# Optimization experiments

Hardware: AMD Instinct MI355X
Metric: run time of the kernel (lower is better)

## Reference

```python
import jax, jax.numpy as jnp
import numpy as np

N_QUBITS = 8
DIM = 2 ** N_QUBITS  # 256


def _apply_1q(state, U, q):
    """Apply a single-qubit gate U on wire q. state: (B, 256) complex64.
    U: (2,2) shared gate or (B,2,2) per-sample gate."""
    B = state.shape[0]
    s = state.reshape(B, 2 ** q, 2, 2 ** (N_QUBITS - 1 - q))
    if U.ndim == 2:
        s = jnp.einsum('ij,bajc->baic', U, s)
    else:
        s = jnp.einsum('bij,bajc->baic', U, s)
    return s.reshape(B, DIM)


def _apply_cnot(state, c, t):
    """CNOT with control wire c, target wire t (pure permutation of amplitudes)."""
    B = state.shape[0]
    a, b = (c, t) if c < t else (t, c)
    s = state.reshape(B, 2 ** a, 2, 2 ** (b - a - 1), 2, 2 ** (N_QUBITS - 1 - b))
    if c < t:
        s0 = s[:, :, 0]                       # control=0: unchanged
        s1 = jnp.flip(s[:, :, 1], axis=3)     # control=1: flip target axis
        s = jnp.stack([s0, s1], axis=2)
    else:
        s0 = s[:, :, :, :, 0]
        s1 = jnp.flip(s[:, :, :, :, 1], axis=2)
        s = jnp.stack([s0, s1], axis=4)
    return s.reshape(B, DIM)


def _rx_batch(theta):
    """Batched RX(theta): (B,) -> (B,2,2) complex64."""
    c = jnp.cos(theta / 2).astype(jnp.complex64)
    s = (-1j * jnp.sin(theta / 2)).astype(jnp.complex64)
    return jnp.stack([jnp.stack([c, s], -1), jnp.stack([s, c], -1)], -2)


def _rot(phi, theta, omega):
    """PennyLane Rot(phi,theta,omega) = RZ(omega) RY(theta) RZ(phi) as a 2x2 matrix."""
    c = jnp.cos(theta / 2)
    s = jnp.sin(theta / 2)
    m00 = jnp.exp(-0.5j * (phi + omega)) * c
    m01 = -jnp.exp(0.5j * (phi - omega)) * s
    m10 = jnp.exp(-0.5j * (phi - omega)) * s
    m11 = jnp.exp(0.5j * (phi + omega)) * c
    return jnp.stack([jnp.stack([m00, m01]), jnp.stack([m10, m11])]).astype(jnp.complex64)


def _circuit(x, weights):
    """AngleEmbedding (RX) + StronglyEntanglingLayers, return <Z_i> per wire: (B,8)."""
    B = x.shape[0]
    state = jnp.zeros((B, DIM), jnp.complex64).at[:, 0].set(1.0)
    # AngleEmbedding: RX(x[:, q]) on wire q
    for q in range(N_QUBITS):
        state = _apply_1q(state, _rx_batch(x[:, q]), q)
    n_layers = weights.shape[0]
    for l in range(n_layers):
        for q in range(N_QUBITS):
            state = _apply_1q(state, _rot(weights[l, q, 0], weights[l, q, 1], weights[l, q, 2]), q)
        r = (l % (N_QUBITS - 1)) + 1  # PennyLane default ranges
        for q in range(N_QUBITS):
            state = _apply_cnot(state, q, (q + r) % N_QUBITS)
    probs = state.real ** 2 + state.imag ** 2  # (B, 256)
    bits = (jnp.arange(DIM)[:, None] >> jnp.arange(N_QUBITS - 1, -1, -1)[None, :]) & 1
    signs = (1.0 - 2.0 * bits).astype(probs.dtype)  # (256, 8); wire 0 = MSB
    return probs @ signs  # (B, 8) expectation values of PauliZ


def setup_inputs() -> dict:
    key = jax.random.key(0)
    k1, k2, k3 = jax.random.split(key, 3)
    B = 32768
    x = jax.random.uniform(k1, (B, N_QUBITS), dtype=jnp.float32)
    weights = jax.random.uniform(k2, (2, N_QUBITS, 3), dtype=jnp.float32, maxval=2.0 * np.pi)
    fc_w = jax.random.normal(k3, (1, N_QUBITS), dtype=jnp.float32) / np.sqrt(N_QUBITS)
    fc_b = jnp.zeros((1,), jnp.float32)
    return {"x": x, "weights": weights, "fc_w": fc_w, "fc_b": fc_b}


def reference(x, weights, fc_w, fc_b):
    z = _circuit(x, weights)                 # (B, 8)
    return jax.nn.sigmoid(z @ fc_w.T + fc_b)  # (B, 1)
```

## Files before the change

kernel.cpp:

```cpp
#include <hip/hip_runtime.h>
#include <hip/hip_fp16.h>
#include <math.h>

#define NQ 8

__host__ __device__ constexpr int cnot_step(int i, int c, int t) {
    return ((i >> (7 - c)) & 1) ? (i ^ (1 << (7 - t))) : i;
}
__host__ __device__ constexpr int sigma_fwd(int i, int r) {
    for (int q = 0; q < 8; ++q) i = cnot_step(i, q, (q + r) & 7);
    return i;
}
__host__ __device__ constexpr int sigma_inv(int i, int r) {
    for (int q = 7; q >= 0; --q) i = cnot_step(i, q, (q + r) & 7);
    return i;
}
__host__ __device__ constexpr int pairmask(int q) { return sigma_inv(1 << (7 - q), 1); }
__host__ __device__ constexpr int rolemask(int q) {
    int m = 0;
    for (int j = 0; j < 8; ++j)
        if ((sigma_fwd(1 << j, 1) >> (7 - q)) & 1) m |= 1 << j;
    return m;
}
__host__ __device__ constexpr int colmask2(int b) {
    return sigma_fwd(sigma_fwd(1 << b, 1), 2);
}

__host__ __device__ constexpr int amp_index(int slot, int k, int hl) {
    return (slot << 7) | (((k >> 2) & 1) << 6) | (((hl >> 3) & 1) << 5)
         | (((hl >> 2) & 1) << 4) | (((hl >> 1) & 1) << 3) | ((hl & 1) << 2)
         | (((k >> 1) & 1) << 1) | (k & 1);
}
__host__ __device__ constexpr int mask_slot(int M) { return (M >> 7) & 1; }
__host__ __device__ constexpr int mask_k(int M) {
    return (((M >> 6) & 1) << 2) | (((M >> 1) & 1) << 1) | (M & 1);
}
__host__ __device__ constexpr int mask_l(int M) { return (M >> 2) & 15; }

typedef _Float16 h2v __attribute__((ext_vector_type(2)));

__device__ __forceinline__ __half2 bc_h2(uint32_t u) { return __builtin_bit_cast(__half2, u); }
__device__ __forceinline__ uint32_t bc_u32(__half2 h) { return __builtin_bit_cast(uint32_t, h); }
__device__ __forceinline__ h2v bc_hv(__half2 h) { return __builtin_bit_cast(h2v, h); }
__device__ __forceinline__ uint32_t rot16(uint32_t u) { return (u >> 16) | (u << 16); }

template<int XM>
__device__ __forceinline__ uint32_t swzu(uint32_t v) {
    return (uint32_t)__builtin_amdgcn_ds_swizzle((int)v, (XM << 10) | 0x1F);
}
template<int XM>
__device__ __forceinline__ float swzf(float v) {
    return __builtin_bit_cast(float, (uint32_t)__builtin_amdgcn_ds_swizzle(
        (int)__builtin_bit_cast(uint32_t, v), (XM << 10) | 0x1F));
}

__device__ __forceinline__ void cmul(float& zr, float& zi,
                                     float xr, float xi, float yr, float yi) {
    const float tr = xr * yr - xi * yi;
    const float ti = xr * yi + xi * yr;
    zr = tr; zi = ti;
}

struct H2C { __half2 re, im; };
__device__ __forceinline__ H2C h2c_mul(H2C x, __half2 yre, __half2 yim, __half2 yimn) {
    H2C z;
    z.re = __hfma2(x.im, yimn, __hmul2(x.re, yre));
    z.im = __hfma2(x.im, yre,  __hmul2(x.re, yim));
    return z;
}

template<int Q>
__device__ __forceinline__ void gateQ(__half2 re[8], __half2 im[8], int hl,
                                      const uint32_t* __restrict__ cw)
{
    constexpr int M  = pairmask(Q);
    constexpr int RM = rolemask(Q);
    constexpr int mk = mask_k(M);
    constexpr int ml = mask_l(M);
    constexpr int ms = mask_slot(M);
    constexpr int rk = mask_k(RM);
    constexpr int rl = mask_l(RM);

    const uint4    c4v = *(const uint4*)(cw + Q * 8);
    const uint32_t WDn = cw[Q * 8 + 4];

    const uint32_t pm = (uint32_t)(__popc(hl & rl) & 1) * 0x80008000u;
    const uint32_t Bp = c4v.y ^ pm, Bn = Bp ^ 0x80008000u;
    const uint32_t Cp = c4v.z ^ pm, Cn = Cp ^ 0x80008000u;
    const __half2  Aw = bc_h2(c4v.x);
    const __half2  Dw = bc_h2(c4v.w);
    const __half2  Dn = bc_h2(WDn);

    auto prep = [](uint32_t v) -> uint32_t {
        if constexpr (ms) v = rot16(v);
        if constexpr (ml) v = swzu<ml>(v);
        return v;
    };
    auto upd = [&](int k, uint32_t pr, uint32_t pi) {
        const bool par = (__popc(k & rk) & 1) != 0;
        const __half2 B1 = bc_h2(par ? Bn : Bp);
        const __half2 B2 = bc_h2(par ? Bp : Bn);
        const __half2 Cc = bc_h2(par ? Cn : Cp);
        __half2 nr = __hmul2(Aw, re[k]);
        nr = __hfma2(B1, im[k], nr);
        nr = __hfma2(Cc, bc_h2(pr), nr);
        nr = __hfma2(Dw, bc_h2(pi), nr);
        __half2 ni = __hmul2(Aw, im[k]);
        ni = __hfma2(B2, re[k], ni);
        ni = __hfma2(Cc, bc_h2(pi), ni);
        ni = __hfma2(Dn, bc_h2(pr), ni);
        re[k] = nr; im[k] = ni;
    };

    if constexpr (mk == 0) {
#pragma unroll
        for (int k = 0; k < 8; ++k) {
            const uint32_t pr = prep(bc_u32(re[k]));
            const uint32_t pi = prep(bc_u32(im[k]));
            upd(k, pr, pi);
        }
    } else {
        constexpr int msb = (mk & 4) ? 4 : ((mk & 2) ? 2 : 1);
#pragma unroll
        for (int k = 0; k < 8; ++k) {
            if ((k & msb) != 0) continue;
            const int k2 = k ^ mk;
            const uint32_t pr_k  = prep(bc_u32(re[k2]));
            const uint32_t pi_k  = prep(bc_u32(im[k2]));
            const uint32_t pr_k2 = prep(bc_u32(re[k]));
            const uint32_t pi_k2 = prep(bc_u32(im[k]));
            upd(k,  pr_k,  pi_k);
            upd(k2, pr_k2, pi_k2);
        }
    }
}

__global__ __launch_bounds__(256, 8) void vqe_fused(
    const float* __restrict__ x,
    const float* __restrict__ weights,
    const float* __restrict__ fc_w,
    const float* __restrict__ fc_b,
    float* __restrict__ out, int B)
{
    __shared__ __align__(16) float    g0[64];
    __shared__ __align__(16) uint32_t cw[64];
    __shared__ __align__(16) float    cols[16 * 36];
    __shared__ __align__(16) uint32_t wth2[16 * 12];

    const int t = threadIdx.x;

    if (t < 8) {
        const float* w3 = weights + t * 3;
        float s, c;   __sincosf(w3[1] * 0.5f, &s, &c);
        float sa, ca; __sincosf(0.5f * (w3[0] + w3[2]), &sa, &ca);
        float sb, cb; __sincosf(0.5f * (w3[0] - w3[2]), &sb, &cb);
        float* g = g0 + t * 8;
        g[0] = c * ca;  g[1] = -c * sa;
        g[2] = -s * cb; g[3] = -s * sb;
        g[4] = s * cb;  g[5] = -s * sb;
        g[6] = c * ca;  g[7] = c * sa;
    } else if (t < 16) {
        const int q = t - 8;
        const float* w3 = weights + (NQ + q) * 3;
        float s, c;   __sincosf(w3[1] * 0.5f, &s, &c);
        float sa, ca; __sincosf(0.5f * (w3[0] + w3[2]), &sa, &ca);
        float sb, cb; __sincosf(0.5f * (w3[0] - w3[2]), &sb, &cb);
        const float A = c * ca, Bc = c * sa, C = s * cb, D = s * sb;
        const float s1 = (rolemask(q) & 0x80) ? -1.f : 1.f;
        uint32_t* cq = cw + q * 8;
        cq[0] = bc_u32(__floats2half2_rn(A, A));
        cq[1] = bc_u32(__floats2half2_rn(Bc, s1 * Bc));
        cq[2] = bc_u32(__floats2half2_rn(-C, -s1 * C));
        cq[3] = bc_u32(__floats2half2_rn(D, D));
        cq[4] = bc_u32(__floats2half2_rn(-D, -D));
        cq[5] = 0; cq[6] = 0; cq[7] = 0;
    } else if (t >= 128) {
        const int tt = t - 128;
        const int whl = tt >> 3, wk = tt & 7;
        float wsl[2];
#pragma unroll
        for (int slot = 0; slot < 2; ++slot) {
            const int s = amp_index(slot, wk, whl);
            int j = 0;
#pragma unroll
            for (int b = 0; b < 8; ++b)
                if ((s >> b) & 1) j ^= colmask2(b);
            float w = 0.f;
#pragma unroll
            for (int q = 0; q < 8; ++q)
                w += ((j >> (7 - q)) & 1) ? -fc_w[q] : fc_w[q];
            wsl[slot] = w;
        }
        wth2[whl * 12 + wk] = bc_u32(__floats2half2_rn(wsl[0], wsl[1]));
    }
    __syncthreads();

    if (t < 128) {
        const int s = t >> 3, q = t & 7;
        const int sg = blockIdx.x * 16 + s;
        if (sg < B) {
            const float xv = x[sg * NQ + q];
            float sn, cs; __sincosf(xv * 0.5f, &sn, &cs);
            const float* g = g0 + q * 8;
            float* c = cols + s * 36 + q * 4;
            c[0] = cs * g[0] + sn * g[3];
            c[1] = cs * g[1] - sn * g[2];
            c[2] = cs * g[4] + sn * g[7];
            c[3] = cs * g[5] - sn * g[6];
        }
    }
    __syncthreads();

    const int lane = t & 63;
    const int hl   = lane & 15;
    const int sidx = ((t >> 6) << 2) | ((lane >> 4) & 3);
    const int samp = blockIdx.x * 16 + sidx;
    if (samp >= B) return;

    const float* cb = cols + sidx * 36;

    const float2 e2 = *(const float2*)(cb + 2 * 4 + ((hl >> 3) & 1) * 2);
    const float2 e3 = *(const float2*)(cb + 3 * 4 + ((hl >> 2) & 1) * 2);
    const float2 e4 = *(const float2*)(cb + 4 * 4 + ((hl >> 1) & 1) * 2);
    const float2 e5 = *(const float2*)(cb + 5 * 4 + (hl & 1) * 2);
    float cr = e2.x, ci = e2.y;
    cmul(cr, ci, cr, ci, e3.x, e3.y);
    cmul(cr, ci, cr, ci, e4.x, e4.y);
    cmul(cr, ci, cr, ci, e5.x, e5.y);

    const float4 c0 = *(const float4*)(cb + 0 * 4);
    const float4 c1 = *(const float4*)(cb + 1 * 4);
    const float4 c6 = *(const float4*)(cb + 6 * 4);
    const float4 c7 = *(const float4*)(cb + 7 * 4);

    float w0r, w0i, w1r, w1i;
    cmul(w0r, w0i, cr, ci, c0.x, c0.y);
    cmul(w1r, w1i, cr, ci, c0.z, c0.w);
    H2C S{__floats2half2_rn(w0r, w1r), __floats2half2_rn(w0i, w1i)};

    const __half2 y7ar = __floats2half2_rn(c7.x, c7.x), y7ai = __floats2half2_rn(c7.y, c7.y);
    const __half2 y7br = __floats2half2_rn(c7.z, c7.z), y7bi = __floats2half2_rn(c7.w, c7.w);
    const __half2 y7ain = bc_h2(bc_u32(y7ai) ^ 0x80008000u);
    const __half2 y7bin = bc_h2(bc_u32(y7bi) ^ 0x80008000u);
    H2C A0 = h2c_mul(S, y7ar, y7ai, y7ain);
    H2C A1 = h2c_mul(S, y7br, y7bi, y7bin);

    const __half2 y6ar = __floats2half2_rn(c6.x, c6.x), y6ai = __floats2half2_rn(c6.y, c6.y);
    const __half2 y6br = __floats2half2_rn(c6.z, c6.z), y6bi = __floats2half2_rn(c6.w, c6.w);
    const __half2 y6ain = bc_h2(bc_u32(y6ai) ^ 0x80008000u);
    const __half2 y6bin = bc_h2(bc_u32(y6bi) ^ 0x80008000u);
    H2C B0 = h2c_mul(A0, y6ar, y6ai, y6ain);
    H2C B1 = h2c_mul(A1, y6ar, y6ai, y6ain);
    H2C B2 = h2c_mul(A0, y6br, y6bi, y6bin);
    H2C B3 = h2c_mul(A1, y6br, y6bi, y6bin);

    const __half2 y1ar = __floats2half2_rn(c1.x, c1.x), y1ai = __floats2half2_rn(c1.y, c1.y);
    const __half2 y1br = __floats2half2_rn(c1.z, c1.z), y1bi = __floats2half2_rn(c1.w, c1.w);
    const __half2 y1ain = bc_h2(bc_u32(y1ai) ^ 0x80008000u);
    const __half2 y1bin = bc_h2(bc_u32(y1bi) ^ 0x80008000u);

    __half2 re[8], im[8];
    {
        H2C z;
        z = h2c_mul(B0, y1ar, y1ai, y1ain); re[0] = z.re; im[0] = z.im;
        z = h2c_mul(B1, y1ar, y1ai, y1ain); re[1] = z.re; im[1] = z.im;
        z = h2c_mul(B2, y1ar, y1ai, y1ain); re[2] = z.re; im[2] = z.im;
        z = h2c_mul(B3, y1ar, y1ai, y1ain); re[3] = z.re; im[3] = z.im;
        z = h2c_mul(B0, y1br, y1bi, y1bin); re[4] = z.re; im[4] = z.im;
        z = h2c_mul(B1, y1br, y1bi, y1bin); re[5] = z.re; im[5] = z.im;
        z = h2c_mul(B2, y1br, y1bi, y1bin); re[6] = z.re; im[6] = z.im;
        z = h2c_mul(B3, y1br, y1bi, y1bin); re[7] = z.re; im[7] = z.im;
    }

    gateQ<0>(re, im, hl, cw);
    gateQ<1>(re, im, hl, cw);
    gateQ<2>(re, im, hl, cw);
    gateQ<3>(re, im, hl, cw);
    gateQ<4>(re, im, hl, cw);
    gateQ<5>(re, im, hl, cw);
    gateQ<6>(re, im, hl, cw);
    gateQ<7>(re, im, hl, cw);

    const uint32_t* wrow = wth2 + hl * 12;
    const uint4 wa = *(const uint4*)(wrow + 0);
    const uint4 wb = *(const uint4*)(wrow + 4);
    const uint32_t wk[8] = {wa.x, wa.y, wa.z, wa.w, wb.x, wb.y, wb.z, wb.w};

    float acc = 0.f;
#pragma unroll
    for (int k = 0; k < 8; ++k) {
        const __half2 W = bc_h2(wk[k]);
        const __half2 tr_ = __hmul2(re[k], W);
        const __half2 ti_ = __hmul2(im[k], W);
#if defined(__has_builtin) && __has_builtin(__builtin_amdgcn_fdot2)
        acc = __builtin_amdgcn_fdot2(bc_hv(tr_), bc_hv(re[k]), acc, false);
        acc = __builtin_amdgcn_fdot2(bc_hv(ti_), bc_hv(im[k]), acc, false);
#else
        acc += __low2float(tr_) * __low2float(re[k]) + __high2float(tr_) * __high2float(re[k]);
        acc += __low2float(ti_) * __low2float(im[k]) + __high2float(ti_) * __high2float(im[k]);
#endif
    }
    acc += swzf<1>(acc);
    acc += swzf<2>(acc);
    acc += swzf<4>(acc);
    acc += swzf<8>(acc);

    if (hl == 0) {
        const float z = acc + fc_b[0];
        out[samp] = 1.0f / (1.0f + __expf(-z));
    }
}

extern "C" void kernel_launch(void* const* d_in, const int* in_sizes, int n_in,
                              void* d_out, int out_size, void* d_ws, size_t ws_size,
                              hipStream_t stream) {
    const float* x       = (const float*)d_in[0];
    const float* weights = (const float*)d_in[1];
    const float* fc_w    = (const float*)d_in[2];
    const float* fc_b    = (const float*)d_in[3];
    float* out = (float*)d_out;

    const int B = in_sizes[0] / NQ;
    const int blocks = (B + 15) / 16;

    vqe_fused<<<blocks, 256, 0, stream>>>(x, weights, fc_w, fc_b, out, B);
}
```

Baseline: 18.79 us.

## Use 8 lanes per sample with 16 amplitudes each and DPP shuffles

Changes the per-sample amplitude layout so each sample is spread over 8 lanes holding 16 half2 amplitude pairs instead of 16 lanes holding 8, doubling samples per block to 32. Lane-exchange masks of 1 and 3 now use DPP quad permutes instead of ds_swizzle, and the final reduction uses three DPP adds instead of four swizzles. The aim is to cut cross-lane traffic and per-sample overhead, at the cost of more registers per thread (launch bounds lowered to 4 waves) and possible occupancy loss.

```diff
diff --git a/kernel.cpp b/kernel.cpp
--- a/kernel.cpp
+++ b/kernel.cpp
@@ -27,15 +27,16 @@
 }
 
 __host__ __device__ constexpr int amp_index(int slot, int k, int hl) {
-    return (slot << 7) | (((k >> 2) & 1) << 6) | (((hl >> 3) & 1) << 5)
-         | (((hl >> 2) & 1) << 4) | (((hl >> 1) & 1) << 3) | ((hl & 1) << 2)
-         | (((k >> 1) & 1) << 1) | (k & 1);
+    return (slot << 7) | (((k >> 3) & 1) << 6) | ((hl & 1) << 5) | (((hl >> 1) & 1) << 4)
+         | (((hl >> 2) & 1) << 3) | (((k >> 2) & 1) << 2) | (((k >> 1) & 1) << 1) | (k & 1);
 }
 __host__ __device__ constexpr int mask_slot(int M) { return (M >> 7) & 1; }
 __host__ __device__ constexpr int mask_k(int M) {
-    return (((M >> 6) & 1) << 2) | (((M >> 1) & 1) << 1) | (M & 1);
-}
-__host__ __device__ constexpr int mask_l(int M) { return (M >> 2) & 15; }
+    return (((M >> 6) & 1) << 3) | (((M >> 2) & 1) << 2) | (((M >> 1) & 1) << 1) | (M & 1);
+}
+__host__ __device__ constexpr int mask_l(int M) {
+    return ((M >> 5) & 1) | (((M >> 4) & 1) << 1) | (((M >> 3) & 1) << 2);
+}
 
 typedef _Float16 h2v __attribute__((ext_vector_type(2)));
 
@@ -48,10 +49,15 @@
 __device__ __forceinline__ uint32_t swzu(uint32_t v) {
     return (uint32_t)__builtin_amdgcn_ds_swizzle((int)v, (XM << 10) | 0x1F);
 }
-template<int XM>
-__device__ __forceinline__ float swzf(float v) {
-    return __builtin_bit_cast(float, (uint32_t)__builtin_amdgcn_ds_swizzle(
-        (int)__builtin_bit_cast(uint32_t, v), (XM << 10) | 0x1F));
+template<int CTRL>
+__device__ __forceinline__ uint32_t dppx(uint32_t v) {
+    return (uint32_t)__builtin_amdgcn_update_dpp(0, (int)v, CTRL, 0xF, 0xF, true);
+}
+template<int CTRL>
+__device__ __forceinline__ float dppaddf(float v) {
+    const uint32_t p = (uint32_t)__builtin_amdgcn_update_dpp(
+        0, (int)__builtin_bit_cast(uint32_t, v), CTRL, 0xF, 0xF, true);
+    return v + __builtin_bit_cast(float, p);
 }
 
 __device__ __forceinline__ void cmul(float& zr, float& zi,
@@ -62,15 +68,23 @@
 }
 
 struct H2C { __half2 re, im; };
-__device__ __forceinline__ H2C h2c_mul(H2C x, __half2 yre, __half2 yim, __half2 yimn) {
+struct YB  { __half2 re, im, imn; };
+__device__ __forceinline__ YB mkyb(float r, float i) {
+    YB y;
+    y.re  = __floats2half2_rn(r, r);
+    y.im  = __floats2half2_rn(i, i);
+    y.imn = bc_h2(bc_u32(y.im) ^ 0x80008000u);
+    return y;
+}
+__device__ __forceinline__ H2C h2c_mul(H2C x, YB y) {
     H2C z;
-    z.re = __hfma2(x.im, yimn, __hmul2(x.re, yre));
-    z.im = __hfma2(x.im, yre,  __hmul2(x.re, yim));
+    z.re = __hfma2(x.im, y.imn, __hmul2(x.re, y.re));
+    z.im = __hfma2(x.im, y.re,  __hmul2(x.re, y.im));
     return z;
 }
 
 template<int Q>
-__device__ __forceinline__ void gateQ(__half2 re[8], __half2 im[8], int hl,
+__device__ __forceinline__ void gateQ(__half2 re[16], __half2 im[16], int hl,
                                       const uint32_t* __restrict__ cw)
 {
     constexpr int M  = pairmask(Q);
@@ -93,7 +107,9 @@
 
     auto prep = [](uint32_t v) -> uint32_t {
         if constexpr (ms) v = rot16(v);
-        if constexpr (ml) v = swzu<ml>(v);
+        if constexpr (ml == 1) v = dppx<0xB1>(v);
+        else if constexpr (ml == 3) v = dppx<0x1B>(v);
+        else if constexpr (ml != 0) v = swzu<ml>(v);
         return v;
     };
     auto upd = [&](int k, uint32_t pr, uint32_t pi) {
@@ -114,15 +130,15 @@
 
     if constexpr (mk == 0) {
 #pragma unroll
-        for (int k = 0; k < 8; ++k) {
+        for (int k = 0; k < 16; ++k) {
             const uint32_t pr = prep(bc_u32(re[k]));
             const uint32_t pi = prep(bc_u32(im[k]));
             upd(k, pr, pi);
         }
     } else {
-        constexpr int msb = (mk & 4) ? 4 : ((mk & 2) ? 2 : 1);
-#pragma unroll
-        for (int k = 0; k < 8; ++k) {
+        constexpr int msb = (mk & 8) ? 8 : ((mk & 4) ? 4 : ((mk & 2) ? 2 : 1));
+#pragma unroll
+        for (int k = 0; k < 16; ++k) {
             if ((k & msb) != 0) continue;
             const int k2 = k ^ mk;
             const uint32_t pr_k  = prep(bc_u32(re[k2]));
@@ -135,7 +151,7 @@
     }
 }
 
-__global__ __launch_bounds__(256, 8) void vqe_fused(
+__global__ __launch_bounds__(256, 4) void vqe_fused(
     const float* __restrict__ x,
     const float* __restrict__ weights,
     const float* __restrict__ fc_w,
@@ -144,8 +160,8 @@
 {
     __shared__ __align__(16) float    g0[64];
     __shared__ __align__(16) uint32_t cw[64];
-    __shared__ __align__(16) float    cols[16 * 36];
-    __shared__ __align__(16) uint32_t wth2[16 * 12];
+    __shared__ __align__(16) float    cols[32 * 36];
+    __shared__ __align__(16) uint32_t wth2[8 * 20];
 
     const int t = threadIdx.x;
 
@@ -176,7 +192,7 @@
         cq[5] = 0; cq[6] = 0; cq[7] = 0;
     } else if (t >= 128) {
         const int tt = t - 128;
-        const int whl = tt >> 3, wk = tt & 7;
+        const int whl = tt >> 4, wk = tt & 15;
         float wsl[2];
 #pragma unroll
         for (int slot = 0; slot < 2; ++slot) {
@@ -191,13 +207,13 @@
                 w += ((j >> (7 - q)) & 1) ? -fc_w[q] : fc_w[q];
             wsl[slot] = w;
         }
-        wth2[whl * 12 + wk] = bc_u32(__floats2half2_rn(wsl[0], wsl[1]));
+        wth2[whl * 20 + wk] = bc_u32(__floats2half2_rn(wsl[0], wsl[1]));
     }
     __syncthreads();
 
-    if (t < 128) {
+    {
         const int s = t >> 3, q = t & 7;
-        const int sg = blockIdx.x * 16 + s;
+        const int sg = blockIdx.x * 32 + s;
         if (sg < B) {
             const float xv = x[sg * NQ + q];
             float sn, cs; __sincosf(xv * 0.5f, &sn, &cs);
@@ -212,24 +228,23 @@
     __syncthreads();
 
     const int lane = t & 63;
-    const int hl   = lane & 15;
-    const int sidx = ((t >> 6) << 2) | ((lane >> 4) & 3);
-    const int samp = blockIdx.x * 16 + sidx;
+    const int hl   = lane & 7;
+    const int sidx = ((t >> 6) << 3) | ((lane >> 3) & 7);
+    const int samp = blockIdx.x * 32 + sidx;
     if (samp >= B) return;
 
     const float* cb = cols + sidx * 36;
 
-    const float2 e2 = *(const float2*)(cb + 2 * 4 + ((hl >> 3) & 1) * 2);
-    const float2 e3 = *(const float2*)(cb + 3 * 4 + ((hl >> 2) & 1) * 2);
-    const float2 e4 = *(const float2*)(cb + 4 * 4 + ((hl >> 1) & 1) * 2);
-    const float2 e5 = *(const float2*)(cb + 5 * 4 + (hl & 1) * 2);
+    const float2 e2 = *(const float2*)(cb + 2 * 4 + (hl & 1) * 2);
+    const float2 e3 = *(const float2*)(cb + 3 * 4 + ((hl >> 1) & 1) * 2);
+    const float2 e4 = *(const float2*)(cb + 4 * 4 + ((hl >> 2) & 1) * 2);
     float cr = e2.x, ci = e2.y;
     cmul(cr, ci, cr, ci, e3.x, e3.y);
     cmul(cr, ci, cr, ci, e4.x, e4.y);
-    cmul(cr, ci, cr, ci, e5.x, e5.y);
 
     const float4 c0 = *(const float4*)(cb + 0 * 4);
     const float4 c1 = *(const float4*)(cb + 1 * 4);
+    const float4 c5 = *(const float4*)(cb + 5 * 4);
     const float4 c6 = *(const float4*)(cb + 6 * 4);
     const float4 c7 = *(const float4*)(cb + 7 * 4);
 
@@ -238,38 +253,29 @@
     cmul(w1r, w1i, cr, ci, c0.z, c0.w);
     H2C S{__floats2half2_rn(w0r, w1r), __floats2half2_rn(w0i, w1i)};
 
-    const __half2 y7ar = __floats2half2_rn(c7.x, c7.x), y7ai = __floats2half2_rn(c7.y, c7.y);
-    const __half2 y7br = __floats2half2_rn(c7.z, c7.z), y7bi = __floats2half2_rn(c7.w, c7.w);
-    const __half2 y7ain = bc_h2(bc_u32(y7ai) ^ 0x80008000u);
-    const __half2 y7bin = bc_h2(bc_u32(y7bi) ^ 0x80008000u);
-    H2C A0 = h2c_mul(S, y7ar, y7ai, y7ain);
-    H2C A1 = h2c_mul(S, y7br, y7bi, y7bin);
-
-    const __half2 y6ar = __floats2half2_rn(c6.x, c6.x), y6ai = __floats2half2_rn(c6.y, c6.y);
-    const __half2 y6br = __floats2half2_rn(c6.z, c6.z), y6bi = __floats2half2_rn(c6.w, c6.w);
-    const __half2 y6ain = bc_h2(bc_u32(y6ai) ^ 0x80008000u);
-    const __half2 y6bin = bc_h2(bc_u32(y6bi) ^ 0x80008000u);
-    H2C B0 = h2c_mul(A0, y6ar, y6ai, y6ain);
-    H2C B1 = h2c_mul(A1, y6ar, y6ai, y6ain);
-    H2C B2 = h2c_mul(A0, y6br, y6bi, y6bin);
-    H2C B3 = h2c_mul(A1, y6br, y6bi, y6bin);
-
-    const __half2 y1ar = __floats2half2_rn(c1.x, c1.x), y1ai = __floats2half2_rn(c1.y, c1.y);
-    const __half2 y1br = __floats2half2_rn(c1.z, c1.z), y1bi = __floats2half2_rn(c1.w, c1.w);
-    const __half2 y1ain = bc_h2(bc_u32(y1ai) ^ 0x80008000u);
-    const __half2 y1bin = bc_h2(bc_u32(y1bi) ^ 0x80008000u);
-
-    __half2 re[8], im[8];
-    {
-        H2C z;
-        z = h2c_mul(B0, y1ar, y1ai, y1ain); re[0] = z.re; im[0] = z.im;
-        z = h2c_mul(B1, y1ar, y1ai, y1ain); re[1] = z.re; im[1] = z.im;
-        z = h2c_mul(B2, y1ar, y1ai, y1ain); re[2] = z.re; im[2] = z.im;
-        z = h2c_mul(B3, y1ar, y1ai, y1ain); re[3] = z.re; im[3] = z.im;
-        z = h2c_mul(B0, y1br, y1bi, y1bin); re[4] = z.re; im[4] = z.im;
-        z = h2c_mul(B1, y1br, y1bi, y1bin); re[5] = z.re; im[5] = z.im;
-        z = h2c_mul(B2, y1br, y1bi, y1bin); re[6] = z.re; im[6] = z.im;
-        z = h2c_mul(B3, y1br, y1bi, y1bin); re[7] = z.re; im[7] = z.im;
+    const YB y1a = mkyb(c1.x, c1.y), y1b = mkyb(c1.z, c1.w);
+    const YB y5a = mkyb(c5.x, c5.y), y5b = mkyb(c5.z, c5.w);
+    const YB y6a = mkyb(c6.x, c6.y), y6b = mkyb(c6.z, c6.w);
+    const YB y7a = mkyb(c7.x, c7.y), y7b = mkyb(c7.z, c7.w);
+
+    const H2C A0 = h2c_mul(S, y1a);
+    const H2C A1 = h2c_mul(S, y1b);
+    H2C Bv[4];
+    Bv[0] = h2c_mul(A0, y5a); Bv[1] = h2c_mul(A0, y5b);
+    Bv[2] = h2c_mul(A1, y5a); Bv[3] = h2c_mul(A1, y5b);
+    H2C Cv[8];
+#pragma unroll
+    for (int j = 0; j < 4; ++j) {
+        Cv[j * 2 + 0] = h2c_mul(Bv[j], y6a);
+        Cv[j * 2 + 1] = h2c_mul(Bv[j], y6b);
+    }
+    __half2 re[16], im[16];
+#pragma unroll
+    for (int j = 0; j < 8; ++j) {
+        const H2C z0 = h2c_mul(Cv[j], y7a);
+        const H2C z1 = h2c_mul(Cv[j], y7b);
+        re[j * 2 + 0] = z0.re; im[j * 2 + 0] = z0.im;
+        re[j * 2 + 1] = z1.re; im[j * 2 + 1] = z1.im;
     }
 
     gateQ<0>(re, im, hl, cw);
@@ -281,15 +287,18 @@
     gateQ<6>(re, im, hl, cw);
     gateQ<7>(re, im, hl, cw);
 
-    const uint32_t* wrow = wth2 + hl * 12;
+    const uint32_t* wrow = wth2 + hl * 20;
     const uint4 wa = *(const uint4*)(wrow + 0);
     const uint4 wb = *(const uint4*)(wrow + 4);
-    const uint32_t wk[8] = {wa.x, wa.y, wa.z, wa.w, wb.x, wb.y, wb.z, wb.w};
+    const uint4 wc = *(const uint4*)(wrow + 8);
+    const uint4 wd = *(const uint4*)(wrow + 12);
+    const uint32_t wkw[16] = {wa.x, wa.y, wa.z, wa.w, wb.x, wb.y, wb.z, wb.w,
+                              wc.x, wc.y, wc.z, wc.w, wd.x, wd.y, wd.z, wd.w};
 
     float acc = 0.f;
 #pragma unroll
-    for (int k = 0; k < 8; ++k) {
-        const __half2 W = bc_h2(wk[k]);
+    for (int k = 0; k < 16; ++k) {
+        const __half2 W = bc_h2(wkw[k]);
         const __half2 tr_ = __hmul2(re[k], W);
         const __half2 ti_ = __hmul2(im[k], W);
 #if defined(__has_builtin) && __has_builtin(__builtin_amdgcn_fdot2)
@@ -300,10 +309,9 @@
         acc += __low2float(ti_) * __low2float(im[k]) + __high2float(ti_) * __high2float(im[k]);
 #endif
     }
-    acc += swzf<1>(acc);
-    acc += swzf<2>(acc);
-    acc += swzf<4>(acc);
-    acc += swzf<8>(acc);
+    acc = dppaddf<0xB1>(acc);
+    acc = dppaddf<0x4E>(acc);
+    acc = dppaddf<0x141>(acc);
 
     if (hl == 0) {
         const float z = acc + fc_b[0];
@@ -319,9 +327,10 @@
     const float* fc_w    = (const float*)d_in[2];
     const float* fc_b    = (const float*)d_in[3];
     float* out = (float*)d_out;
+    (void)d_ws; (void)ws_size;
 
     const int B = in_sizes[0] / NQ;
-    const int blocks = (B + 15) / 16;
+    const int blocks = (B + 31) / 32;
 
     vqe_fused<<<blocks, 256, 0, stream>>>(x, weights, fc_w, fc_b, out, B);
 }
```

Measured after the change: 18.12 us. 1.04x faster.
